# Optimization experiments

Measured on AMD Instinct MI355X. Metric: run time of the kernel, lower is better.

## Reference

```python
import jax, jax.numpy as jnp
import numpy as np

K = 20
EPS = 1e-5
NEG_SLOPE = 0.2


def _bn(x, g, b, m, v, axis):
    # inference batchnorm over channel axis
    shape = [1] * x.ndim
    shape[axis] = -1
    inv = g * jax.lax.rsqrt(v + EPS)
    return x * inv.reshape(shape) + (b - m * inv).reshape(shape)


def _lrelu(x):
    return jnp.where(x >= 0, x, NEG_SLOPE * x)


def _graph_feature(x, k):
    # x: (B, C, N) -> (B, 2C, N, k)
    B, C, N = x.shape
    xt = jnp.swapaxes(x, 1, 2)                      # (B, N, C)
    inner = -2.0 * jnp.einsum('bnc,bmc->bnm', xt, xt)
    xx = jnp.sum(xt * xt, axis=-1)                  # (B, N)
    pairwise = -xx[:, :, None] - inner - xx[:, None, :]  # (B, N, N) = -||xi-xj||^2
    _, idx = jax.lax.top_k(pairwise, k)             # (B, N, k)
    # gather neighbor features: (B, N, k, C)
    neigh = jnp.take_along_axis(xt[:, None, :, :], idx[:, :, :, None], axis=2)
    center = xt[:, :, None, :]                      # (B, N, 1, C)
    feat = jnp.concatenate([neigh - center, jnp.broadcast_to(center, neigh.shape)], axis=-1)
    return jnp.transpose(feat, (0, 3, 1, 2))        # (B, 2C, N, k)


def setup_inputs() -> dict:
    key = jax.random.key(0)
    ks = jax.random.split(key, 24)
    B, C, N = 8, 64, 4096
    d = {
        'x': jax.random.normal(ks[0], (B, C, N), jnp.float32),
        'w_k1': jax.random.normal(ks[1], (64, 128), jnp.float32) * 0.05,
        'g_k1': jax.random.uniform(ks[2], (64,), jnp.float32),
        'b_k1': jax.random.normal(ks[3], (64,), jnp.float32) * 0.05,
        'm_k1': jax.random.normal(ks[4], (64,), jnp.float32) * 0.05,
        'v_k1': jax.random.uniform(ks[5], (64,), jnp.float32) + 0.5,
        'w_k2': jax.random.normal(ks[6], (64, 64), jnp.float32) * 0.05,
        'g_k2': jax.random.uniform(ks[7], (64,), jnp.float32),
        'b_k2': jax.random.normal(ks[8], (64,), jnp.float32) * 0.05,
        'm_k2': jax.random.normal(ks[9], (64,), jnp.float32) * 0.05,
        'v_k2': jax.random.uniform(ks[10], (64,), jnp.float32) + 0.5,
        'w1': jax.random.normal(ks[11], (256, 64), jnp.float32) * 0.05,
        'g1': jax.random.uniform(ks[12], (256,), jnp.float32),
        'b1': jax.random.normal(ks[13], (256,), jnp.float32) * 0.05,
        'm1': jax.random.normal(ks[14], (256,), jnp.float32) * 0.05,
        'v1': jax.random.uniform(ks[15], (256,), jnp.float32) + 0.5,
        'w2': jax.random.normal(ks[16], (128, 256), jnp.float32) * 0.05,
        'g2': jax.random.uniform(ks[17], (128,), jnp.float32),
        'b2': jax.random.normal(ks[18], (128,), jnp.float32) * 0.05,
        'm2': jax.random.normal(ks[19], (128,), jnp.float32) * 0.05,
        'v2': jax.random.uniform(ks[20], (128,), jnp.float32) + 0.5,
        'w3': jax.random.normal(ks[21], (1, 128), jnp.float32) * 0.05,
        'b3': jax.random.normal(ks[22], (1,), jnp.float32) * 0.05,
    }
    return d


def reference(x, w_k1, g_k1, b_k1, m_k1, v_k1, w_k2, g_k2, b_k2, m_k2, v_k2,
              w1, g1, b1, m1, v1, w2, g2, b2, m2, v2, w3, b3):
    # kNN edge features: (B, 2C, N, k)
    f = _graph_feature(x, K)
    # EdgeConv blocks: 1x1 conv2d (bias=False) + BN + LeakyReLU
    f = _lrelu(_bn(jnp.einsum('oc,bcnk->bonk', w_k1, f), g_k1, b_k1, m_k1, v_k1, 1))
    f = _lrelu(_bn(jnp.einsum('oc,bcnk->bonk', w_k2, f), g_k2, b_k2, m_k2, v_k2, 1))
    h = jnp.max(f, axis=-1)                         # (B, 64, N) amax over neighbors
    h = _lrelu(_bn(jnp.einsum('oc,bcn->bon', w1, h), g1, b1, m1, v1, 1))
    h = _lrelu(_bn(jnp.einsum('oc,bcn->bon', w2, h), g2, b2, m2, v2, 1))
    # dropout is identity in eval mode
    out = jnp.einsum('oc,bcn->bon', w3, h) + b3[None, :, None]  # (B, 1, N)
    return out.squeeze(axis=-2)                     # (B, N)
```

## Files before the change

### kernel.cpp

```cpp
#include <hip/hip_runtime.h>
#include <hip/hip_bf16.h>

#define B_ 8
#define C_ 64
#define N_ 4096
#define K_ 20
#define EPS_ 1e-5f
#define SLOPE_ 0.2f

typedef __attribute__((ext_vector_type(8))) short bf16x8;
typedef __attribute__((ext_vector_type(4))) float f32x4;

__device__ __forceinline__ float lrelu(float x) { return x >= 0.f ? x : SLOPE_ * x; }
__device__ __forceinline__ float bf2f(unsigned short u) {
    return __uint_as_float(((unsigned int)u) << 16);
}
__device__ __forceinline__ unsigned short f2bf(float f) {
    unsigned int u = __float_as_uint(f);
    return (unsigned short)((u + 0x7FFFu + ((u >> 16) & 1u)) >> 16);
}

__device__ __forceinline__ float rdlanef(float x, int l) {
    return __int_as_float(__builtin_amdgcn_readlane(__float_as_int(x), l));
}

__global__ void __launch_bounds__(256) k_pre(const float* __restrict__ x,
                                             const float* __restrict__ wk1,
                                             float* __restrict__ yA,
                                             float* __restrict__ dd,
                                             float* __restrict__ xx,
                                             unsigned short* __restrict__ xps) {
    __shared__ float xs[64][64];
    __shared__ unsigned short wimg[16384];
    __shared__ unsigned short ximg[8192];
    int t = threadIdx.x;
    int lane = t & 63;
    int w = t >> 6;
    int blk = blockIdx.x;
    int b = blk >> 6;
    int n0 = (blk & 63) << 6;

    const float* xb = x + (size_t)b * C_ * N_;
    for (int i = 0; i < 4; ++i) {
        int j = i * 256 + t;
        int c = j >> 4;
        int p4 = (j & 15) << 2;
        float4 v = *(const float4*)(xb + c * N_ + n0 + p4);
        xs[c][p4 + 0] = v.x; xs[c][p4 + 1] = v.y;
        xs[c][p4 + 2] = v.z; xs[c][p4 + 3] = v.w;
    }
    for (int rep = 0; rep < 4; ++rep) {
        int i = rep * 256 + t;
        int m = i >> 3, oct = i & 7;
        const float* src = wk1 + (m & 63) * 128 + ((m >> 6) << 6) + oct * 8;
        float4 a4 = *(const float4*)src;
        float4 b4 = *(const float4*)(src + 4);
        float wv[8] = {a4.x, a4.y, a4.z, a4.w, b4.x, b4.y, b4.z, b4.w};
        bf16x8 hv, lv8;
#pragma unroll
        for (int j = 0; j < 8; ++j) {
            unsigned short hh = f2bf(wv[j]);
            hv[j] = (short)hh;
            lv8[j] = (short)f2bf(wv[j] - bf2f(hh));
        }
        int unit = oct ^ (m & 7);
        *(bf16x8*)&wimg[m * 64 + unit * 8] = hv;
        *(bf16x8*)&wimg[8192 + m * 64 + unit * 8] = lv8;
    }
    __syncthreads();

    if (t < 64) {
        float s = 0.f;
        for (int c = 0; c < 64; ++c) { float xv = xs[c][t]; s += xv * xv; }
        xx[b * N_ + n0 + t] = s;
    }

    unsigned short* xc = xps + ((size_t)(b * 64 + (blk & 63))) * 8192;
#pragma unroll
    for (int q = 0; q < 2; ++q) {
        int i = q * 256 + t;
        int nl = i >> 3, oct = i & 7;
        bf16x8 hv, lv8;
#pragma unroll
        for (int j = 0; j < 8; ++j) {
            float v = xs[oct * 8 + j][nl];
            unsigned short hh = f2bf(v);
            hv[j] = (short)hh;
            lv8[j] = (short)f2bf(v - bf2f(hh));
        }
        int unit = oct ^ (nl & 7);
        *(bf16x8*)&ximg[nl * 64 + unit * 8] = hv;
        *(bf16x8*)&ximg[4096 + nl * 64 + unit * 8] = lv8;
        *(bf16x8*)&xc[nl * 64 + unit * 8] = hv;
        *(bf16x8*)&xc[4096 + nl * 64 + unit * 8] = lv8;
    }
    __syncthreads();

    int mA = (w << 4) + (lane & 15);
    int mB = ((w + 4) << 4) + (lane & 15);
    bf16x8 ahA[2], alA[2], ahB[2], alB[2];
#pragma unroll
    for (int kc = 0; kc < 2; ++kc) {
        int uA = (kc * 4 + (lane >> 4)) ^ (mA & 7);
        int uB = (kc * 4 + (lane >> 4)) ^ (mB & 7);
        ahA[kc] = *(const bf16x8*)&wimg[mA * 64 + uA * 8];
        alA[kc] = *(const bf16x8*)&wimg[8192 + mA * 64 + uA * 8];
        ahB[kc] = *(const bf16x8*)&wimg[mB * 64 + uB * 8];
        alB[kc] = *(const bf16x8*)&wimg[8192 + mB * 64 + uB * 8];
    }
    size_t pbase = (size_t)(b * N_ + n0);
#pragma unroll
    for (int nt = 0; nt < 4; ++nt) {
        int p = nt * 16 + (lane & 15);
        int u0 = ((lane >> 4)) ^ (p & 7);
        int u1 = (4 + (lane >> 4)) ^ (p & 7);
        bf16x8 bh0 = *(const bf16x8*)&ximg[p * 64 + u0 * 8];
        bf16x8 bl0 = *(const bf16x8*)&ximg[4096 + p * 64 + u0 * 8];
        bf16x8 bh1 = *(const bf16x8*)&ximg[p * 64 + u1 * 8];
        bf16x8 bl1 = *(const bf16x8*)&ximg[4096 + p * 64 + u1 * 8];
        f32x4 aA = {0.f, 0.f, 0.f, 0.f};
        aA = __builtin_amdgcn_mfma_f32_16x16x32_bf16(ahA[0], bh0, aA, 0, 0, 0);
        aA = __builtin_amdgcn_mfma_f32_16x16x32_bf16(ahA[0], bl0, aA, 0, 0, 0);
        aA = __builtin_amdgcn_mfma_f32_16x16x32_bf16(alA[0], bh0, aA, 0, 0, 0);
        aA = __builtin_amdgcn_mfma_f32_16x16x32_bf16(alA[0], bl0, aA, 0, 0, 0);
        aA = __builtin_amdgcn_mfma_f32_16x16x32_bf16(ahA[1], bh1, aA, 0, 0, 0);
        aA = __builtin_amdgcn_mfma_f32_16x16x32_bf16(ahA[1], bl1, aA, 0, 0, 0);
        aA = __builtin_amdgcn_mfma_f32_16x16x32_bf16(alA[1], bh1, aA, 0, 0, 0);
        aA = __builtin_amdgcn_mfma_f32_16x16x32_bf16(alA[1], bl1, aA, 0, 0, 0);
        f32x4 aB = {0.f, 0.f, 0.f, 0.f};
        aB = __builtin_amdgcn_mfma_f32_16x16x32_bf16(ahB[0], bh0, aB, 0, 0, 0);
        aB = __builtin_amdgcn_mfma_f32_16x16x32_bf16(ahB[0], bl0, aB, 0, 0, 0);
        aB = __builtin_amdgcn_mfma_f32_16x16x32_bf16(alB[0], bh0, aB, 0, 0, 0);
        aB = __builtin_amdgcn_mfma_f32_16x16x32_bf16(alB[0], bl0, aB, 0, 0, 0);
        aB = __builtin_amdgcn_mfma_f32_16x16x32_bf16(ahB[1], bh1, aB, 0, 0, 0);
        aB = __builtin_amdgcn_mfma_f32_16x16x32_bf16(ahB[1], bl1, aB, 0, 0, 0);
        aB = __builtin_amdgcn_mfma_f32_16x16x32_bf16(alB[1], bh1, aB, 0, 0, 0);
        aB = __builtin_amdgcn_mfma_f32_16x16x32_bf16(alB[1], bl1, aB, 0, 0, 0);

        int obase = (w << 4) + ((lane >> 4) << 2);
        float4 ya4 = {aA[0], aA[1], aA[2], aA[3]};
        float4 dd4 = {aB[0] - aA[0], aB[1] - aA[1], aB[2] - aA[2], aB[3] - aA[3]};
        *(float4*)(yA + (pbase + p) * 64 + obase) = ya4;
        *(float4*)(dd + (pbase + p) * 64 + obase) = dd4;
    }
}

__global__ void __launch_bounds__(512) k_topk(const unsigned short* __restrict__ xps,
                                              const float* __restrict__ xx,
                                              int* __restrict__ idxg) {
    __shared__ float sc[2][32][68];
    int t = threadIdx.x;
    int lane = t & 63;
    int w = t >> 6;
    int wr = w >> 2;
    int wc = w & 3;
    int blk = blockIdx.x;
    int b = blk >> 7;
    int n0 = (blk & 127) << 5;
    int bc = b << 6;
    const float* xxb = xx + b * N_;
    int pa = ((lane + 1) & 63) << 2;

    const unsigned short* xcA = xps + ((size_t)(bc + ((blk & 127) >> 1))) * 8192;
    int anl = ((blk & 1) << 5) + (wr << 4) + (lane & 15);
    bf16x8 ah[2], al[2];
#pragma unroll
    for (int kc = 0; kc < 2; ++kc) {
        int unit = (kc * 4 + (lane >> 4)) ^ (anl & 7);
        ah[kc] = *(const bf16x8*)&xcA[anl * 64 + unit * 8];
        al[kc] = *(const bf16x8*)&xcA[4096 + anl * 64 + unit * 8];
    }

    int n_ = (wc << 4) + (lane & 15);
    int off0 = n_ * 64 + (((lane >> 4)) ^ (n_ & 7)) * 8;
    int off1 = n_ * 64 + ((4 + (lane >> 4)) ^ (n_ & 7)) * 8;

    float lv[4];
    int   li[4];
#pragma unroll
    for (int i = 0; i < 4; ++i) { lv[i] = -3.0e38f; li[i] = 0; }

    auto ins = [&](float& lvr, int& lir, float s, int m0) {
        float mnc = rdlanef(lvr, 19);
        unsigned long long mask = __ballot(s > mnc);
        while (mask) {
            int j = (int)__builtin_ctzll(mask);
            mask &= mask - 1;
            float sv = rdlanef(s, j);
            unsigned long long gt = __ballot(lane < 20 && lvr > sv);
            int cpos = __popcll(gt);
            float upv = __int_as_float(
                __builtin_amdgcn_ds_permute(pa, __float_as_int(lvr)));
            int   upi = __builtin_amdgcn_ds_permute(pa, lir);
            if (lane >= cpos && lane < 20) {
                lvr = (lane == cpos) ? sv : upv;
                lir = (lane == cpos) ? (m0 + j) : upi;
            }
        }
    };

    const unsigned short* xcB = xps + (size_t)bc * 8192;
    bf16x8 bh0 = *(const bf16x8*)&xcB[off0];
    bf16x8 bl0 = *(const bf16x8*)&xcB[4096 + off0];
    bf16x8 bh1 = *(const bf16x8*)&xcB[off1];
    bf16x8 bl1 = *(const bf16x8*)&xcB[4096 + off1];
    float xxv = xxb[n_];

    for (int mc = 0; mc < 64; ++mc) {
        f32x4 acc = {0.f, 0.f, 0.f, 0.f};
        acc = __builtin_amdgcn_mfma_f32_16x16x32_bf16(ah[0], bh0, acc, 0, 0, 0);
        acc = __builtin_amdgcn_mfma_f32_16x16x32_bf16(ah[0], bl0, acc, 0, 0, 0);
        acc = __builtin_amdgcn_mfma_f32_16x16x32_bf16(al[0], bh0, acc, 0, 0, 0);
        acc = __builtin_amdgcn_mfma_f32_16x16x32_bf16(al[0], bl0, acc, 0, 0, 0);
        acc = __builtin_amdgcn_mfma_f32_16x16x32_bf16(ah[1], bh1, acc, 0, 0, 0);
        acc = __builtin_amdgcn_mfma_f32_16x16x32_bf16(ah[1], bl1, acc, 0, 0, 0);
        acc = __builtin_amdgcn_mfma_f32_16x16x32_bf16(al[1], bh1, acc, 0, 0, 0);
        acc = __builtin_amdgcn_mfma_f32_16x16x32_bf16(al[1], bl1, acc, 0, 0, 0);

#pragma unroll
        for (int r = 0; r < 4; ++r)
            sc[mc & 1][(wr << 4) + ((lane >> 4) << 2) + r][n_] = 2.f * acc[r] - xxv;

        if (mc + 1 < 64) {
            const unsigned short* xn2 = xps + (size_t)(bc + mc + 1) * 8192;
            bh0 = *(const bf16x8*)&xn2[off0];
            bl0 = *(const bf16x8*)&xn2[4096 + off0];
            bh1 = *(const bf16x8*)&xn2[off1];
            bl1 = *(const bf16x8*)&xn2[4096 + off1];
            xxv = xxb[((mc + 1) << 6) + n_];
        }

        if (mc > 0) {
            int m0p = (mc - 1) << 6;
#pragma unroll
            for (int i = 0; i < 4; ++i) {
                int lrow = (w << 2) + i;
                float s = sc[(mc - 1) & 1][lrow][lane];
                ins(lv[i], li[i], s, m0p);
            }
        }
        __syncthreads();
    }

    {
        int m0p = 63 << 6;
#pragma unroll
        for (int i = 0; i < 4; ++i) {
            int lrow = (w << 2) + i;
            float s = sc[1][lrow][lane];
            ins(lv[i], li[i], s, m0p);
        }
    }

#pragma unroll
    for (int i = 0; i < 4; ++i) {
        int n = n0 + (w << 2) + i;
        if (lane < K_)
            idxg[((size_t)(b * N_ + n)) * K_ + lane] = li[i];
    }
}

__global__ void __launch_bounds__(256) k_edge(const float* __restrict__ yA,
                                              const float* __restrict__ dd,
                                              const int* __restrict__ idxg,
                                              const float* __restrict__ wk2,
                                              const float* __restrict__ g1,
                                              const float* __restrict__ bb1,
                                              const float* __restrict__ mm1,
                                              const float* __restrict__ vv1,
                                              const float* __restrict__ g2,
                                              const float* __restrict__ bb2,
                                              const float* __restrict__ mm2,
                                              const float* __restrict__ vv2,
                                              float* __restrict__ ht) {
    __shared__ unsigned short wimg[8192];
    __shared__ float ubuf[64 * 164];
    __shared__ float s1c[64], t1c[64], s2c[64], t2c[64];
    __shared__ float ddl[8][64];
    __shared__ int   il[8][K_];
    __shared__ float hl[8][64];
    unsigned short* timgH = (unsigned short*)ubuf;
    unsigned short* timgL = timgH + 160 * 64;
    float* ct = ubuf;

    int t = threadIdx.x;
    int lane = t & 63;
    int w = t >> 6;
    int blk = blockIdx.x;
    int b = blk >> 9;
    int n0 = (blk & 511) << 3;

    for (int rep = 0; rep < 2; ++rep) {
        int i = rep * 256 + t;
        int row = i >> 3, oct = i & 7;
        float4 wa = *(const float4*)(wk2 + row * 64 + oct * 8);
        float4 wb = *(const float4*)(wk2 + row * 64 + oct * 8 + 4);
        float wv[8] = {wa.x, wa.y, wa.z, wa.w, wb.x, wb.y, wb.z, wb.w};
        bf16x8 hv, lv8;
#pragma unroll
        for (int j = 0; j < 8; ++j) {
            unsigned short hh = f2bf(wv[j]);
            hv[j] = (short)hh;
            lv8[j] = (short)f2bf(wv[j] - bf2f(hh));
        }
        int unit = oct ^ (row & 7);
        *(bf16x8*)&wimg[row * 64 + unit * 8] = hv;
        *(bf16x8*)&wimg[4096 + row * 64 + unit * 8] = lv8;
    }
    if (t < 64) {
        float g = g1[t], be = bb1[t], m = mm1[t], v = vv1[t];
        float s = g * rsqrtf(v + EPS_);
        s1c[t] = s; t1c[t] = be - m * s;
        g = g2[t]; be = bb2[t]; m = mm2[t]; v = vv2[t];
        s = g * rsqrtf(v + EPS_);
        s2c[t] = s; t2c[t] = be - m * s;
    }
    size_t pbase = (size_t)(b * N_ + n0);
    for (int i = t; i < 512; i += 256) {
        int pt = i >> 6, o = i & 63;
        ddl[pt][o] = dd[(pbase + pt) * 64 + o];
    }
    if (t < 8 * K_) {
        int pt = t / K_, k = t % K_;
        il[pt][k] = idxg[(pbase + pt) * K_ + k];
    }
    __syncthreads();

    const float* yAb = yA + (size_t)(b * N_) * 64;
    float4 ga[5][2];
    int gcol[5], goct[5], gpt[5];
#pragma unroll
    for (int rep = 0; rep < 5; ++rep) {
        int j = rep * 256 + t;
        int pt = j / 160;
        int r = j - pt * 160;
        int k = r >> 3, oct = r & 7;
        int m = il[pt][k];
        const float* src = yAb + (size_t)m * 64 + oct * 8;
        ga[rep][0] = *(const float4*)src;
        ga[rep][1] = *(const float4*)(src + 4);
        gcol[rep] = pt * 20 + k; goct[rep] = oct; gpt[rep] = pt;
    }
#pragma unroll
    for (int rep = 0; rep < 5; ++rep) {
        int oct = goct[rep], pt = gpt[rep], col = gcol[rep];
        float yv[8] = {ga[rep][0].x, ga[rep][0].y, ga[rep][0].z, ga[rep][0].w,
                       ga[rep][1].x, ga[rep][1].y, ga[rep][1].z, ga[rep][1].w};
        bf16x8 hv, lv8;
#pragma unroll
        for (int jj = 0; jj < 8; ++jj) {
            int oc = oct * 8 + jj;
            float v = lrelu(s1c[oc] * (yv[jj] + ddl[pt][oc]) + t1c[oc]);
            unsigned short hh = f2bf(v);
            hv[jj] = (short)hh;
            lv8[jj] = (short)f2bf(v - bf2f(hh));
        }
        int unit = oct ^ (col & 7);
        *(bf16x8*)&timgH[col * 64 + unit * 8] = hv;
        *(bf16x8*)&timgL[col * 64 + unit * 8] = lv8;
    }
    __syncthreads();

    int anl = (w << 4) + (lane & 15);
    bf16x8 ah[2], al[2];
#pragma unroll
    for (int kc = 0; kc < 2; ++kc) {
        int unit = (kc * 4 + (lane >> 4)) ^ (anl & 7);
        ah[kc] = *(const bf16x8*)&wimg[anl * 64 + unit * 8];
        al[kc] = *(const bf16x8*)&wimg[4096 + anl * 64 + unit * 8];
    }
    f32x4 acc[10];
#pragma unroll
    for (int nt = 0; nt < 10; ++nt) {
        int col = nt * 16 + (lane & 15);
        int u0 = ((lane >> 4)) ^ (col & 7);
        int u1 = (4 + (lane >> 4)) ^ (col & 7);
        bf16x8 bh0 = *(const bf16x8*)&timgH[col * 64 + u0 * 8];
        bf16x8 bl0 = *(const bf16x8*)&timgL[col * 64 + u0 * 8];
        bf16x8 bh1 = *(const bf16x8*)&timgH[col * 64 + u1 * 8];
        bf16x8 bl1 = *(const bf16x8*)&timgL[col * 64 + u1 * 8];
        f32x4 a = {0.f, 0.f, 0.f, 0.f};
        a = __builtin_amdgcn_mfma_f32_16x16x32_bf16(ah[0], bh0, a, 0, 0, 0);
        a = __builtin_amdgcn_mfma_f32_16x16x32_bf16(ah[0], bl0, a, 0, 0, 0);
        a = __builtin_amdgcn_mfma_f32_16x16x32_bf16(al[0], bh0, a, 0, 0, 0);
        a = __builtin_amdgcn_mfma_f32_16x16x32_bf16(al[0], bl0, a, 0, 0, 0);
        a = __builtin_amdgcn_mfma_f32_16x16x32_bf16(ah[1], bh1, a, 0, 0, 0);
        a = __builtin_amdgcn_mfma_f32_16x16x32_bf16(ah[1], bl1, a, 0, 0, 0);
        a = __builtin_amdgcn_mfma_f32_16x16x32_bf16(al[1], bh1, a, 0, 0, 0);
        a = __builtin_amdgcn_mfma_f32_16x16x32_bf16(al[1], bl1, a, 0, 0, 0);
        acc[nt] = a;
    }
    __syncthreads();

#pragma unroll
    for (int nt = 0; nt < 10; ++nt) {
#pragma unroll
        for (int r = 0; r < 4; ++r)
            ct[((w << 4) + ((lane >> 4) << 2) + r) * 164 + nt * 16 + (lane & 15)] =
                acc[nt][r];
    }
    __syncthreads();

#pragma unroll
    for (int rep = 0; rep < 2; ++rep) {
        int pair = rep * 256 + t;
        int o2 = pair >> 3, pt = pair & 7;
        const float* row = &ct[o2 * 164 + pt * 20];
        float4 c0 = *(const float4*)(row + 0);
        float4 c1 = *(const float4*)(row + 4);
        float4 c2 = *(const float4*)(row + 8);
        float4 c3 = *(const float4*)(row + 12);
        float4 c4 = *(const float4*)(row + 16);
        float mx = fmaxf(fmaxf(fmaxf(c0.x, c0.y), fmaxf(c0.z, c0.w)),
                   fmaxf(fmaxf(fmaxf(c1.x, c1.y), fmaxf(c1.z, c1.w)),
                   fmaxf(fmaxf(fmaxf(c2.x, c2.y), fmaxf(c2.z, c2.w)),
                   fmaxf(fmaxf(fmaxf(c3.x, c3.y), fmaxf(c3.z, c3.w)),
                         fmaxf(fmaxf(c4.x, c4.y), fmaxf(c4.z, c4.w))))));
        hl[pt][o2] = lrelu(s2c[o2] * mx + t2c[o2]);
    }
    __syncthreads();

    float* htb = ht + (size_t)b * 64 * N_;
    for (int i = t; i < 512; i += 256) {
        int o = i >> 3, pt2 = i & 7;
        htb[o * N_ + n0 + pt2] = hl[pt2][o];
    }
}

__global__ void __launch_bounds__(256) k_head(const float* __restrict__ ht,
                                              const float* __restrict__ w1,
                                              const float* __restrict__ g1,
                                              const float* __restrict__ bb1,
                                              const float* __restrict__ mm1,
                                              const float* __restrict__ vv1,
                                              const float* __restrict__ w2,
                                              const float* __restrict__ g2,
                                              const float* __restrict__ bb2,
                                              const float* __restrict__ mm2,
                                              const float* __restrict__ vv2,
                                              const float* __restrict__ w3,
                                              const float* __restrict__ b3,
                                              float* __restrict__ out) {
    __shared__ float hbuf[64][64];
    __shared__ float a1[256][64];
    __shared__ float a2[128][64];
    __shared__ float sA[256], tA[256], sB[128], tB[128];
    int t = threadIdx.x;
    int blk = blockIdx.x;
    int b = blk >> 6;
    int n0 = (blk & 63) << 6;
    const float* htb = ht + (size_t)b * 64 * N_;

    for (int i = 0; i < 16; ++i) {
        int j = i * 256 + t;
        int o = j >> 6, pt = j & 63;
        hbuf[o][pt] = htb[o * N_ + n0 + pt];
    }
    {
        float g = g1[t], be = bb1[t], m = mm1[t], v = vv1[t];
        float s = g * rsqrtf(v + EPS_);
        sA[t] = s; tA[t] = be - m * s;
    }
    if (t < 128) {
        float g = g2[t], be = bb2[t], m = mm2[t], v = vv2[t];
        float s = g * rsqrtf(v + EPS_);
        sB[t] = s; tB[t] = be - m * s;
    }
    __syncthreads();

    int ptg = t & 15, rg = t >> 4;
    int pt4 = ptg << 2;

    for (int ib = 0; ib < 4; ++ib) {
        int r0 = (rg << 4) + (ib << 2);
        float acc[4][4] = {};
        for (int o4 = 0; o4 < 16; ++o4) {
            float hf[4][4];
            for (int c = 0; c < 4; ++c) {
                float4 q = *(const float4*)&hbuf[(o4 << 2) + c][pt4];
                hf[c][0] = q.x; hf[c][1] = q.y; hf[c][2] = q.z; hf[c][3] = q.w;
            }
            for (int j = 0; j < 4; ++j) {
                float4 wv4 = *(const float4*)(w1 + (r0 + j) * 64 + (o4 << 2));
                float wv[4] = {wv4.x, wv4.y, wv4.z, wv4.w};
                for (int c = 0; c < 4; ++c)
                    for (int pp = 0; pp < 4; ++pp)
                        acc[j][pp] += wv[c] * hf[c][pp];
            }
        }
        for (int j = 0; j < 4; ++j) {
            int r = r0 + j;
            float4 ov;
            ov.x = lrelu(sA[r] * acc[j][0] + tA[r]);
            ov.y = lrelu(sA[r] * acc[j][1] + tA[r]);
            ov.z = lrelu(sA[r] * acc[j][2] + tA[r]);
            ov.w = lrelu(sA[r] * acc[j][3] + tA[r]);
            *(float4*)&a1[r][pt4] = ov;
        }
    }
    __syncthreads();

    for (int ib = 0; ib < 2; ++ib) {
        int r0 = (rg << 3) + (ib << 2);
        float acc[4][4] = {};
        for (int p4i = 0; p4i < 64; ++p4i) {
            float af[4][4];
            for (int c = 0; c < 4; ++c) {
                float4 q = *(const float4*)&a1[(p4i << 2) + c][pt4];
                af[c][0] = q.x; af[c][1] = q.y; af[c][2] = q.z; af[c][3] = q.w;
            }
            for (int j = 0; j < 4; ++j) {
                float4 wv4 = *(const float4*)(w2 + (r0 + j) * 256 + (p4i << 2));
                float wv[4] = {wv4.x, wv4.y, wv4.z, wv4.w};
                for (int c = 0; c < 4; ++c)
                    for (int pp = 0; pp < 4; ++pp)
                        acc[j][pp] += wv[c] * af[c][pp];
            }
        }
        for (int j = 0; j < 4; ++j) {
            int r = r0 + j;
            float4 ov;
            ov.x = lrelu(sB[r] * acc[j][0] + tB[r]);
            ov.y = lrelu(sB[r] * acc[j][1] + tB[r]);
            ov.z = lrelu(sB[r] * acc[j][2] + tB[r]);
            ov.w = lrelu(sB[r] * acc[j][3] + tB[r]);
            *(float4*)&a2[r][pt4] = ov;
        }
    }
    __syncthreads();

    if (t < 64) {
        float accv = 0.f;
        for (int q = 0; q < 128; ++q) accv += w3[q] * a2[q][t];
        accv += b3[0];
        out[b * N_ + n0 + t] = accv;
    }
}

extern "C" void kernel_launch(void* const* d_in, const int* in_sizes, int n_in,
                              void* d_out, int out_size, void* d_ws, size_t ws_size,
                              hipStream_t stream) {
    (void)in_sizes; (void)n_in; (void)out_size; (void)ws_size;
    const float* x    = (const float*)d_in[0];
    const float* wk1  = (const float*)d_in[1];
    const float* gk1  = (const float*)d_in[2];
    const float* bk1  = (const float*)d_in[3];
    const float* mk1  = (const float*)d_in[4];
    const float* vk1  = (const float*)d_in[5];
    const float* wk2  = (const float*)d_in[6];
    const float* gk2  = (const float*)d_in[7];
    const float* bk2  = (const float*)d_in[8];
    const float* mk2  = (const float*)d_in[9];
    const float* vk2  = (const float*)d_in[10];
    const float* w1   = (const float*)d_in[11];
    const float* g1   = (const float*)d_in[12];
    const float* b1   = (const float*)d_in[13];
    const float* m1   = (const float*)d_in[14];
    const float* v1   = (const float*)d_in[15];
    const float* w2   = (const float*)d_in[16];
    const float* g2   = (const float*)d_in[17];
    const float* b2   = (const float*)d_in[18];
    const float* m2   = (const float*)d_in[19];
    const float* v2   = (const float*)d_in[20];
    const float* w3   = (const float*)d_in[21];
    const float* b3   = (const float*)d_in[22];

    char* ws = (char*)d_ws;
    float* yA  = (float*)(ws);
    float* dd  = (float*)(ws + 8388608);
    float* xx  = (float*)(ws + 16777216);
    int*   idx = (int*)  (ws + 16908288);
    float* ht  = (float*)(ws + 19529728);
    unsigned short* xps = (unsigned short*)(ws + 27918336);

    k_pre <<<B_ * (N_ / 64), 256, 0, stream>>>(x, wk1, yA, dd, xx, xps);
    k_topk<<<B_ * (N_ / 32), 512, 0, stream>>>(xps, xx, idx);
    k_edge<<<B_ * (N_ / 8),  256, 0, stream>>>(yA, dd, idx, wk2,
                                               gk1, bk1, mk1, vk1,
                                               gk2, bk2, mk2, vk2, ht);
    k_head<<<B_ * (N_ / 64), 256, 0, stream>>>(ht, w1, g1, b1, m1, v1,
                                               w2, g2, b2, m2, v2, w3, b3,
                                               (float*)d_out);
}
```

Baseline: 341.4 us.

## Move head MLP matmuls to split-bf16 MFMA with fused final projection

The point-wise head kernel (64->256->128->1) used scalar FP32 FMAs over shared-memory tiles. It now splits activations and weights into high and low bf16 parts and runs both layers on 16x16x32 MFMA instructions with three or four cross products, chunking the 256-wide hidden layer in two halves to cut LDS use. The final 128->1 projection is fused into the accumulator epilogue with lane shuffles and a small cross-wave reduction. A shared split8 helper also replaces repeated inline loops elsewhere. The trade is extra conversion work and a small precision risk in exchange for matrix-core throughput.

```diff
diff --git a/kernel.cpp b/kernel.cpp
--- a/kernel.cpp
+++ b/kernel.cpp
@@ -22,6 +22,15 @@
 
 __device__ __forceinline__ float rdlanef(float x, int l) {
     return __int_as_float(__builtin_amdgcn_readlane(__float_as_int(x), l));
+}
+
+__device__ __forceinline__ void split8(const float* v, bf16x8& h, bf16x8& l) {
+#pragma unroll
+    for (int j = 0; j < 8; ++j) {
+        unsigned short hh = f2bf(v[j]);
+        h[j] = (short)hh;
+        l[j] = (short)f2bf(v[j] - bf2f(hh));
+    }
 }
 
 __global__ void __launch_bounds__(256) k_pre(const float* __restrict__ x,
@@ -57,12 +66,7 @@
         float4 b4 = *(const float4*)(src + 4);
         float wv[8] = {a4.x, a4.y, a4.z, a4.w, b4.x, b4.y, b4.z, b4.w};
         bf16x8 hv, lv8;
-#pragma unroll
-        for (int j = 0; j < 8; ++j) {
-            unsigned short hh = f2bf(wv[j]);
-            hv[j] = (short)hh;
-            lv8[j] = (short)f2bf(wv[j] - bf2f(hh));
-        }
+        split8(wv, hv, lv8);
         int unit = oct ^ (m & 7);
         *(bf16x8*)&wimg[m * 64 + unit * 8] = hv;
         *(bf16x8*)&wimg[8192 + m * 64 + unit * 8] = lv8;
@@ -80,14 +84,11 @@
     for (int q = 0; q < 2; ++q) {
         int i = q * 256 + t;
         int nl = i >> 3, oct = i & 7;
+        float wv[8];
+#pragma unroll
+        for (int j = 0; j < 8; ++j) wv[j] = xs[oct * 8 + j][nl];
         bf16x8 hv, lv8;
-#pragma unroll
-        for (int j = 0; j < 8; ++j) {
-            float v = xs[oct * 8 + j][nl];
-            unsigned short hh = f2bf(v);
-            hv[j] = (short)hh;
-            lv8[j] = (short)f2bf(v - bf2f(hh));
-        }
+        split8(wv, hv, lv8);
         int unit = oct ^ (nl & 7);
         *(bf16x8*)&ximg[nl * 64 + unit * 8] = hv;
         *(bf16x8*)&ximg[4096 + nl * 64 + unit * 8] = lv8;
@@ -297,12 +298,7 @@
         float4 wb = *(const float4*)(wk2 + row * 64 + oct * 8 + 4);
         float wv[8] = {wa.x, wa.y, wa.z, wa.w, wb.x, wb.y, wb.z, wb.w};
         bf16x8 hv, lv8;
-#pragma unroll
-        for (int j = 0; j < 8; ++j) {
-            unsigned short hh = f2bf(wv[j]);
-            hv[j] = (short)hh;
-            lv8[j] = (short)f2bf(wv[j] - bf2f(hh));
-        }
+        split8(wv, hv, lv8);
         int unit = oct ^ (row & 7);
         *(bf16x8*)&wimg[row * 64 + unit * 8] = hv;
         *(bf16x8*)&wimg[4096 + row * 64 + unit * 8] = lv8;
@@ -346,15 +342,14 @@
         int oct = goct[rep], pt = gpt[rep], col = gcol[rep];
         float yv[8] = {ga[rep][0].x, ga[rep][0].y, ga[rep][0].z, ga[rep][0].w,
                        ga[rep][1].x, ga[rep][1].y, ga[rep][1].z, ga[rep][1].w};
-        bf16x8 hv, lv8;
+        float tv[8];
 #pragma unroll
         for (int jj = 0; jj < 8; ++jj) {
             int oc = oct * 8 + jj;
-            float v = lrelu(s1c[oc] * (yv[jj] + ddl[pt][oc]) + t1c[oc]);
-            unsigned short hh = f2bf(v);
-            hv[jj] = (short)hh;
-            lv8[jj] = (short)f2bf(v - bf2f(hh));
-        }
+            tv[jj] = lrelu(s1c[oc] * (yv[jj] + ddl[pt][oc]) + t1c[oc]);
+        }
+        bf16x8 hv, lv8;
+        split8(tv, hv, lv8);
         int unit = oct ^ (col & 7);
         *(bf16x8*)&timgH[col * 64 + unit * 8] = hv;
         *(bf16x8*)&timgL[col * 64 + unit * 8] = lv8;
@@ -441,20 +436,29 @@
                                               const float* __restrict__ w3,
                                               const float* __restrict__ b3,
                                               float* __restrict__ out) {
-    __shared__ float hbuf[64][64];
-    __shared__ float a1[256][64];
-    __shared__ float a2[128][64];
-    __shared__ float sA[256], tA[256], sB[128], tB[128];
+    __shared__ unsigned int himgH[64 * 36];
+    __shared__ unsigned int himgL[64 * 36];
+    __shared__ float a1f[64 * 132];
+    __shared__ float sA[256], tA[256], sB[128], tB[128], w3s[128];
+    __shared__ float outp[4][64];
     int t = threadIdx.x;
+    int lane = t & 63;
+    int w = t >> 6;
     int blk = blockIdx.x;
     int b = blk >> 6;
     int n0 = (blk & 63) << 6;
     const float* htb = ht + (size_t)b * 64 * N_;
 
-    for (int i = 0; i < 16; ++i) {
-        int j = i * 256 + t;
-        int o = j >> 6, pt = j & 63;
-        hbuf[o][pt] = htb[o * N_ + n0 + pt];
+#pragma unroll
+    for (int rep = 0; rep < 8; ++rep) {
+        int i = rep * 256 + t;
+        int pt = i & 63, op = i >> 6;
+        float v0 = htb[(2 * op) * N_ + n0 + pt];
+        float v1 = htb[(2 * op + 1) * N_ + n0 + pt];
+        unsigned short h0 = f2bf(v0), h1 = f2bf(v1);
+        unsigned short l0 = f2bf(v0 - bf2f(h0)), l1 = f2bf(v1 - bf2f(h1));
+        himgH[pt * 36 + op] = (unsigned int)h0 | ((unsigned int)h1 << 16);
+        himgL[pt * 36 + op] = (unsigned int)l0 | ((unsigned int)l1 << 16);
     }
     {
         float g = g1[t], be = bb1[t], m = mm1[t], v = vv1[t];
@@ -465,76 +469,121 @@
         float g = g2[t], be = bb2[t], m = mm2[t], v = vv2[t];
         float s = g * rsqrtf(v + EPS_);
         sB[t] = s; tB[t] = be - m * s;
-    }
-    __syncthreads();
-
-    int ptg = t & 15, rg = t >> 4;
-    int pt4 = ptg << 2;
-
-    for (int ib = 0; ib < 4; ++ib) {
-        int r0 = (rg << 4) + (ib << 2);
-        float acc[4][4] = {};
-        for (int o4 = 0; o4 < 16; ++o4) {
-            float hf[4][4];
-            for (int c = 0; c < 4; ++c) {
-                float4 q = *(const float4*)&hbuf[(o4 << 2) + c][pt4];
-                hf[c][0] = q.x; hf[c][1] = q.y; hf[c][2] = q.z; hf[c][3] = q.w;
-            }
-            for (int j = 0; j < 4; ++j) {
-                float4 wv4 = *(const float4*)(w1 + (r0 + j) * 64 + (o4 << 2));
-                float wv[4] = {wv4.x, wv4.y, wv4.z, wv4.w};
-                for (int c = 0; c < 4; ++c)
-                    for (int pp = 0; pp < 4; ++pp)
-                        acc[j][pp] += wv[c] * hf[c][pp];
-            }
-        }
-        for (int j = 0; j < 4; ++j) {
-            int r = r0 + j;
-            float4 ov;
-            ov.x = lrelu(sA[r] * acc[j][0] + tA[r]);
-            ov.y = lrelu(sA[r] * acc[j][1] + tA[r]);
-            ov.z = lrelu(sA[r] * acc[j][2] + tA[r]);
-            ov.w = lrelu(sA[r] * acc[j][3] + tA[r]);
-            *(float4*)&a1[r][pt4] = ov;
-        }
-    }
-    __syncthreads();
-
-    for (int ib = 0; ib < 2; ++ib) {
-        int r0 = (rg << 3) + (ib << 2);
-        float acc[4][4] = {};
-        for (int p4i = 0; p4i < 64; ++p4i) {
-            float af[4][4];
-            for (int c = 0; c < 4; ++c) {
-                float4 q = *(const float4*)&a1[(p4i << 2) + c][pt4];
-                af[c][0] = q.x; af[c][1] = q.y; af[c][2] = q.z; af[c][3] = q.w;
-            }
-            for (int j = 0; j < 4; ++j) {
-                float4 wv4 = *(const float4*)(w2 + (r0 + j) * 256 + (p4i << 2));
-                float wv[4] = {wv4.x, wv4.y, wv4.z, wv4.w};
-                for (int c = 0; c < 4; ++c)
-                    for (int pp = 0; pp < 4; ++pp)
-                        acc[j][pp] += wv[c] * af[c][pp];
-            }
-        }
-        for (int j = 0; j < 4; ++j) {
-            int r = r0 + j;
-            float4 ov;
-            ov.x = lrelu(sB[r] * acc[j][0] + tB[r]);
-            ov.y = lrelu(sB[r] * acc[j][1] + tB[r]);
-            ov.z = lrelu(sB[r] * acc[j][2] + tB[r]);
-            ov.w = lrelu(sB[r] * acc[j][3] + tB[r]);
-            *(float4*)&a2[r][pt4] = ov;
-        }
-    }
-    __syncthreads();
-
-    if (t < 64) {
-        float accv = 0.f;
-        for (int q = 0; q < 128; ++q) accv += w3[q] * a2[q][t];
-        accv += b3[0];
-        out[b * N_ + n0 + t] = accv;
-    }
+        w3s[t] = w3[t];
+    }
+    __syncthreads();
+
+    f32x4 acc2[2][4];
+#pragma unroll
+    for (int i = 0; i < 2; ++i)
+#pragma unroll
+        for (int j = 0; j < 4; ++j) acc2[i][j] = (f32x4){0.f, 0.f, 0.f, 0.f};
+
+    for (int ka = 0; ka < 2; ++ka) {
+        bf16x8 wh[2][2], wl[2][2];
+#pragma unroll
+        for (int mtl2 = 0; mtl2 < 2; ++mtl2) {
+            int mabs = 128 * ka + ((2 * w + mtl2) << 4) + (lane & 15);
+#pragma unroll
+            for (int kc = 0; kc < 2; ++kc) {
+                const float* p = w1 + mabs * 64 + kc * 32 + ((lane >> 4) << 3);
+                float4 q0 = *(const float4*)p;
+                float4 q1 = *(const float4*)(p + 4);
+                float vv8[8] = {q0.x, q0.y, q0.z, q0.w, q1.x, q1.y, q1.z, q1.w};
+                split8(vv8, wh[mtl2][kc], wl[mtl2][kc]);
+            }
+        }
+#pragma unroll
+        for (int nt = 0; nt < 4; ++nt) {
+            int pt = (nt << 4) + (lane & 15);
+            f32x4 aAcc[2] = {{0.f, 0.f, 0.f, 0.f}, {0.f, 0.f, 0.f, 0.f}};
+#pragma unroll
+            for (int kc = 0; kc < 2; ++kc) {
+                int chb = kc * 32 + ((lane >> 4) << 3);
+                bf16x8 bh = *(const bf16x8*)((const unsigned short*)himgH + pt * 72 + chb);
+                bf16x8 bl = *(const bf16x8*)((const unsigned short*)himgL + pt * 72 + chb);
+#pragma unroll
+                for (int mtl2 = 0; mtl2 < 2; ++mtl2) {
+                    aAcc[mtl2] = __builtin_amdgcn_mfma_f32_16x16x32_bf16(wh[mtl2][kc], bh, aAcc[mtl2], 0, 0, 0);
+                    aAcc[mtl2] = __builtin_amdgcn_mfma_f32_16x16x32_bf16(wh[mtl2][kc], bl, aAcc[mtl2], 0, 0, 0);
+                    aAcc[mtl2] = __builtin_amdgcn_mfma_f32_16x16x32_bf16(wl[mtl2][kc], bh, aAcc[mtl2], 0, 0, 0);
+                    aAcc[mtl2] = __builtin_amdgcn_mfma_f32_16x16x32_bf16(wl[mtl2][kc], bl, aAcc[mtl2], 0, 0, 0);
+                }
+            }
+#pragma unroll
+            for (int mtl2 = 0; mtl2 < 2; ++mtl2) {
+                int klocal = ((2 * w + mtl2) << 4) + ((lane >> 4) << 2);
+                int rabs = 128 * ka + klocal;
+                float4 ov;
+                ov.x = lrelu(sA[rabs + 0] * aAcc[mtl2][0] + tA[rabs + 0]);
+                ov.y = lrelu(sA[rabs + 1] * aAcc[mtl2][1] + tA[rabs + 1]);
+                ov.z = lrelu(sA[rabs + 2] * aAcc[mtl2][2] + tA[rabs + 2]);
+                ov.w = lrelu(sA[rabs + 3] * aAcc[mtl2][3] + tA[rabs + 3]);
+                *(float4*)&a1f[pt * 132 + klocal] = ov;
+            }
+        }
+        __syncthreads();
+
+#pragma unroll
+        for (int kc2 = 0; kc2 < 4; ++kc2) {
+            bf16x8 ah2[2], al2[2];
+#pragma unroll
+            for (int mt2 = 0; mt2 < 2; ++mt2) {
+                int oabs = (w << 5) + (mt2 << 4) + (lane & 15);
+                const float* p = w2 + oabs * 256 + 128 * ka + kc2 * 32 + ((lane >> 4) << 3);
+                float4 q0 = *(const float4*)p;
+                float4 q1 = *(const float4*)(p + 4);
+                float vv8[8] = {q0.x, q0.y, q0.z, q0.w, q1.x, q1.y, q1.z, q1.w};
+                split8(vv8, ah2[mt2], al2[mt2]);
+            }
+#pragma unroll
+            for (int nt = 0; nt < 4; ++nt) {
+                int pt = (nt << 4) + (lane & 15);
+                int kl = kc2 * 32 + ((lane >> 4) << 3);
+                float4 q0 = *(const float4*)&a1f[pt * 132 + kl];
+                float4 q1 = *(const float4*)&a1f[pt * 132 + kl + 4];
+                float vv8[8] = {q0.x, q0.y, q0.z, q0.w, q1.x, q1.y, q1.z, q1.w};
+                bf16x8 bh, bl;
+                split8(vv8, bh, bl);
+#pragma unroll
+                for (int mt2 = 0; mt2 < 2; ++mt2) {
+                    acc2[mt2][nt] = __builtin_amdgcn_mfma_f32_16x16x32_bf16(ah2[mt2], bh, acc2[mt2][nt], 0, 0, 0);
+                    acc2[mt2][nt] = __builtin_amdgcn_mfma_f32_16x16x32_bf16(ah2[mt2], bl, acc2[mt2][nt], 0, 0, 0);
+                    acc2[mt2][nt] = __builtin_amdgcn_mfma_f32_16x16x32_bf16(al2[mt2], bh, acc2[mt2][nt], 0, 0, 0);
+                    acc2[mt2][nt] = __builtin_amdgcn_mfma_f32_16x16x32_bf16(al2[mt2], bl, acc2[mt2][nt], 0, 0, 0);
+                }
+            }
+        }
+        __syncthreads();
+    }
+
+    float part[4] = {0.f, 0.f, 0.f, 0.f};
+#pragma unroll
+    for (int mt2 = 0; mt2 < 2; ++mt2) {
+        int ob = (w << 5) + (mt2 << 4) + ((lane >> 4) << 2);
+#pragma unroll
+        for (int nt = 0; nt < 4; ++nt) {
+#pragma unroll
+            for (int r = 0; r < 4; ++r) {
+                int o = ob + r;
+                float a2v = lrelu(sB[o] * acc2[mt2][nt][r] + tB[o]);
+                part[nt] += w3s[o] * a2v;
+            }
+        }
+    }
+#pragma unroll
+    for (int nt = 0; nt < 4; ++nt) {
+        part[nt] += __shfl_xor(part[nt], 16);
+        part[nt] += __shfl_xor(part[nt], 32);
+    }
+    if (lane < 16) {
+#pragma unroll
+        for (int nt = 0; nt < 4; ++nt)
+            outp[w][(nt << 4) + lane] = part[nt];
+    }
+    __syncthreads();
+    if (t < 64)
+        out[b * N_ + n0 + t] = outp[0][t] + outp[1][t] + outp[2][t] + outp[3][t] + b3[0];
 }
 
 extern "C" void kernel_launch(void* const* d_in, const int* in_sizes, int n_in,
```

After: 301.3 us. -11.7%, faster.
